# Kernel tuning notes

Measured on AMD Instinct MI355X. Metric: run time of the kernel, lower is better.

The kernel has to match this reference:

```python
import jax, jax.numpy as jnp
import numpy as np

NEG_SLOPE = 0.2  # PyG GATConv default negative_slope


def setup_inputs() -> dict:
    key = jax.random.key(0)
    ks = jax.random.split(key, 6)
    N, E, IN, H, C = 100000, 1600000, 128, 4, 32
    x = jax.random.normal(ks[0], (N, IN), dtype=jnp.float32)
    edge_index = jax.random.randint(ks[1], (2, E), 0, N, dtype=jnp.int64)
    W = jax.random.normal(ks[2], (IN, H * C), dtype=jnp.float32) * (1.0 / np.sqrt(IN))
    att_src = jax.random.normal(ks[3], (H, C), dtype=jnp.float32) * 0.1
    att_dst = jax.random.normal(ks[4], (H, C), dtype=jnp.float32) * 0.1
    bias = jax.random.normal(ks[5], (H * C,), dtype=jnp.float32) * 0.01
    return {"x": x, "edge_index": edge_index, "W": W,
            "att_src": att_src, "att_dst": att_dst, "bias": bias}


def reference(x, edge_index, W, att_src, att_dst, bias):
    N = x.shape[0]
    H, C = att_src.shape
    # PyG GATConv default add_self_loops=True
    loops = jnp.arange(N, dtype=edge_index.dtype)
    src = jnp.concatenate([edge_index[0], loops])  # [Et]
    dst = jnp.concatenate([edge_index[1], loops])  # [Et]
    # shared linear transform (GATConv uses one lin when in_channels is int)
    h = (x @ W).reshape(N, H, C)                   # [N,H,C]
    a_src = jnp.einsum('nhc,hc->nh', h, att_src)   # [N,H]
    a_dst = jnp.einsum('nhc,hc->nh', h, att_dst)   # [N,H]
    # edge attention logits + leaky relu
    e = jax.nn.leaky_relu(a_src[src] + a_dst[dst], NEG_SLOPE)  # [Et,H]
    # segment softmax over incoming edges of each destination node
    m = jax.ops.segment_max(e, dst, num_segments=N)            # [N,H]
    p = jnp.exp(e - m[dst])                                    # [Et,H]
    denom = jax.ops.segment_sum(p, dst, num_segments=N)        # [N,H]
    alpha = p / denom[dst]                                     # [Et,H]
    # weighted message passing: gather src features, scale, scatter-add to dst
    msg = h[src] * alpha[:, :, None]                           # [Et,H,C]
    out = jax.ops.segment_sum(msg, dst, num_segments=N)        # [N,H,C]
    out = out.reshape(N, H * C) + bias                         # concat heads + bias
    return jax.nn.elu(out)                                     # block ELU (dropout off)
```

## Files before the change

### kernel.cpp

```cpp
#include <hip/hip_runtime.h>
#include <hip/hip_bf16.h>

#define NEG_SLOPE 0.2f
#define BCAP 5120u

typedef __attribute__((ext_vector_type(8))) short bf16x8;
typedef __attribute__((ext_vector_type(4))) float f32x4;

__device__ __forceinline__ float lrelu(float v) { return v > 0.0f ? v : NEG_SLOPE * v; }

__device__ __forceinline__ unsigned bf16pair(float a, float b) {
    unsigned ua = __float_as_uint(a), ub = __float_as_uint(b);
    ua = (ua + 0x7FFFu + ((ua >> 16) & 1u)) >> 16;
    ub = (ub + 0x7FFFu + ((ub >> 16) & 1u)) >> 16;
    return ua | (ub << 16);
}

__device__ __forceinline__ void gload16(const void* g, void* l) {
    __builtin_amdgcn_global_load_lds(
        (const __attribute__((address_space(1))) unsigned*)g,
        (__attribute__((address_space(3))) unsigned*)l, 16, 0, 0);
}

__global__ __launch_bounds__(256) void k_wt(const float* __restrict__ W,
                                            unsigned short* __restrict__ Wt) {
    int gid = blockIdx.x * 256 + threadIdx.x;
    int col = gid >> 7, k = gid & 127;
    float v = W[(size_t)k * 128 + col];
    unsigned u = __float_as_uint(v);
    u = (u + 0x7FFFu + ((u >> 16) & 1u)) >> 16;
    Wt[col * 128 + k] = (unsigned short)u;
}

__global__ __launch_bounds__(512) void k_gembk(const float* __restrict__ x,
                                               const unsigned short* __restrict__ Wt,
                                               const float* __restrict__ att_src,
                                               const float* __restrict__ att_dst,
                                               unsigned* __restrict__ hb,
                                               float* __restrict__ a_src,
                                               float* __restrict__ a_dst,
                                               const int* __restrict__ ei,
                                               unsigned* __restrict__ gcur,
                                               unsigned* __restrict__ ebuf,
                                               int N, int E, int NB, int NBK, int EPB) {
    __shared__ unsigned char sm[65536];
    int t = threadIdx.x;

    if ((int)blockIdx.x < NBK) {
        unsigned* cnt = (unsigned*)sm;
        unsigned* cur2 = (unsigned*)(sm + 2048);
        unsigned* lbase = (unsigned*)(sm + 4096);
        int base = blockIdx.x * EPB;
        int lim = base + EPB;
        if (lim > E) lim = E;
        for (int j = t; j < NB; j += 512) { cnt[j] = 0u; cur2[j] = 0u; }
        __syncthreads();
        for (int i = base + t; i < lim; i += 512)
            atomicAdd(&cnt[(unsigned)ei[(size_t)E + i] >> 8], 1u);
        __syncthreads();
        for (int j = t; j < NB; j += 512) {
            unsigned c = cnt[j];
            lbase[j] = c ? ((unsigned)j * BCAP + atomicAdd(&gcur[j], c)) : 0u;
        }
        __syncthreads();
        for (int i = base + t; i < lim; i += 512) {
            unsigned s = (unsigned)ei[i];
            unsigned d = (unsigned)ei[(size_t)E + i];
            unsigned b = d >> 8;
            unsigned k = atomicAdd(&cur2[b], 1u);
            unsigned slot = lbase[b] + k;
            if (slot < (b + 1u) * BCAP) ebuf[slot] = s | ((d & 255u) << 24);
        }
        return;
    }

    unsigned char* smA = sm;
    unsigned char* smB = sm + 32768;
    int w = t >> 6, lane = t & 63;
    int row0 = ((int)blockIdx.x - NBK) * 128;

#pragma unroll
    for (int it = 0; it < 4; ++it) {
        int L = it * 512 + t;
        int r = L >> 4, c = L & 15;
        int gr = row0 + r;
        if (gr >= N) gr = N - 1;
        float4 f0 = ((const float4*)x)[(size_t)gr * 32 + c * 2];
        float4 f1 = ((const float4*)x)[(size_t)gr * 32 + c * 2 + 1];
        uint4 u;
        u.x = bf16pair(f0.x, f0.y);
        u.y = bf16pair(f0.z, f0.w);
        u.z = bf16pair(f1.x, f1.y);
        u.w = bf16pair(f1.z, f1.w);
        *(uint4*)&smA[r * 256 + ((c ^ (r & 7)) * 16)] = u;
    }
#pragma unroll
    for (int it = 0; it < 4; ++it) {
        int L = w * 256 + it * 64 + lane;
        int r = L >> 4, c = L & 15;
        int cg = c ^ (r & 7);
        gload16((const unsigned*)Wt + r * 64 + cg * 4, smB + (size_t)w * 4096 + it * 1024);
    }
    __syncthreads();

    int lr = lane & 15, lg = lane >> 4;
    int ar = w * 16 + lr;

    f32x4 acc[8];
#pragma unroll
    for (int j = 0; j < 8; ++j)
#pragma unroll
        for (int q = 0; q < 4; ++q) acc[j][q] = 0.f;

#pragma unroll
    for (int kc = 0; kc < 4; ++kc) {
        bf16x8 av = *(const bf16x8*)&smA[ar * 256 + (((kc * 4 + lg) ^ (ar & 7)) * 16)];
        bf16x8 bv[8];
#pragma unroll
        for (int cf = 0; cf < 8; ++cf) {
            int bc = cf * 16 + lr;
            bv[cf] = *(const bf16x8*)&smB[bc * 256 + (((kc * 4 + lg) ^ (bc & 7)) * 16)];
        }
#pragma unroll
        for (int cf = 0; cf < 8; ++cf)
            acc[cf] = __builtin_amdgcn_mfma_f32_16x16x32_bf16(av, bv[cf], acc[cf], 0, 0, 0);
    }

    float att_s[8], att_d[8];
#pragma unroll
    for (int cf = 0; cf < 8; ++cf) {
        att_s[cf] = att_src[cf * 16 + lr];
        att_d[cf] = att_dst[cf * 16 + lr];
    }
#pragma unroll
    for (int reg = 0; reg < 4; ++reg) {
        int row = row0 + w * 16 + lg * 4 + reg;
        float ps[4], pd[4];
#pragma unroll
        for (int hh = 0; hh < 4; ++hh) {
            ps[hh] = acc[2 * hh][reg] * att_s[2 * hh] + acc[2 * hh + 1][reg] * att_s[2 * hh + 1];
            pd[hh] = acc[2 * hh][reg] * att_d[2 * hh] + acc[2 * hh + 1][reg] * att_d[2 * hh + 1];
        }
#pragma unroll
        for (int m = 1; m <= 8; m <<= 1) {
#pragma unroll
            for (int hh = 0; hh < 4; ++hh) {
                ps[hh] += __shfl_xor(ps[hh], m);
                pd[hh] += __shfl_xor(pd[hh], m);
            }
        }
        if (lr == 0 && row < N) {
            ((float4*)a_src)[row] = float4{ps[0], ps[1], ps[2], ps[3]};
            ((float4*)a_dst)[row] = float4{pd[0], pd[1], pd[2], pd[3]};
        }
    }

    unsigned char* scratch = smA + (size_t)w * 4096;
#pragma unroll
    for (int cf = 0; cf < 8; ++cf) {
#pragma unroll
        for (int reg = 0; reg < 4; ++reg) {
            float v = acc[cf][reg];
            float vo = __shfl_xor(v, 1);
            if (!(lane & 1))
                *(unsigned*)&scratch[(lg * 4 + reg) * 256 + cf * 32 + (lr >> 1) * 4] =
                    bf16pair(v, vo);
        }
    }
#pragma unroll
    for (int q = 0; q < 4; ++q) {
        uint4 u = *(const uint4*)&scratch[q * 1024 + lane * 16];
        int row = row0 + w * 16 + q * 4 + lg;
        if (row < N) ((uint4*)hb)[(size_t)row * 16 + lr] = u;
    }
}

__global__ __launch_bounds__(512) void k_scanB(const unsigned* __restrict__ gcur,
                                               unsigned* __restrict__ blockScan, int NB) {
    __shared__ unsigned s[512];
    int t = threadIdx.x;
    unsigned v = (t < NB) ? min(gcur[t], BCAP) : 0u;
    s[t] = v;
    __syncthreads();
    for (int off = 1; off < 512; off <<= 1) {
        unsigned a = (t >= off) ? s[t - off] : 0u;
        __syncthreads();
        s[t] += a;
        __syncthreads();
    }
    if (t < NB) blockScan[t] = s[t] - v;
}

__global__ __launch_bounds__(256) void k_place(const unsigned* __restrict__ ebuf,
                                               const unsigned* __restrict__ gcur,
                                               const unsigned* __restrict__ blockScan,
                                               unsigned* __restrict__ deg,
                                               unsigned* __restrict__ part,
                                               unsigned* __restrict__ csr_src) {
    __shared__ unsigned cnt[256];
    __shared__ unsigned sc[256];
    __shared__ unsigned excl[256];
    __shared__ unsigned curL[256];
    int t = threadIdx.x;
    int b = blockIdx.x;
    cnt[t] = 0u;
    curL[t] = 0u;
    __syncthreads();
    unsigned total = min(gcur[b], BCAP);
    unsigned rbase = (unsigned)b * BCAP;
    for (unsigned i = t; i < total; i += 256)
        atomicAdd(&cnt[ebuf[rbase + i] >> 24], 1u);
    __syncthreads();
    unsigned v = cnt[t];
    sc[t] = v;
    __syncthreads();
    for (int off = 1; off < 256; off <<= 1) {
        unsigned a = (t >= off) ? sc[t - off] : 0u;
        __syncthreads();
        sc[t] += a;
        __syncthreads();
    }
    excl[t] = sc[t] - v;
    deg[b * 256 + t] = v;
    part[b * 256 + t] = sc[t] - v;
    __syncthreads();
    unsigned wbase = blockScan[b];
    for (unsigned i = t; i < total; i += 256) {
        unsigned e = ebuf[rbase + i];
        unsigned dLow = e >> 24;
        unsigned r = atomicAdd(&curL[dLow], 1u);
        csr_src[wbase + excl[dLow] + r] = e & 0x00FFFFFFu;
    }
}

__global__ __launch_bounds__(256) void k_gather(const uint4* __restrict__ hb4,
                                                const unsigned* __restrict__ csr_src,
                                                const unsigned* __restrict__ part,
                                                const unsigned* __restrict__ blockScan,
                                                const unsigned* __restrict__ deg,
                                                const float* __restrict__ a_src,
                                                const float* __restrict__ a_dst,
                                                const float* __restrict__ bias,
                                                float* __restrict__ out, int N) {
    int n = (int)((blockIdx.x * 256 + threadIdx.x) >> 6);
    int lane = threadIdx.x & 63;
    if (n >= N) return;
    int g = lane >> 4;
    int L = lane & 15;
    int head = L >> 2;
    unsigned off = part[n] + blockScan[n >> 8];
    unsigned end = off + deg[n];
    float ad_n = a_dst[n * 4 + head];
    float acc[8];
#pragma unroll
    for (int i = 0; i < 8; ++i) acc[i] = 0.f;
    float dsum = 0.f;
    for (unsigned b = off; b < end; b += 8) {
        unsigned sidx = csr_src[min(b + (unsigned)(lane & 7), end - 1)];
#pragma unroll
        for (int sub = 0; sub < 2; ++sub) {
            int eidx = sub * 4 + g;
            unsigned s = (unsigned)__shfl((int)sidx, eidx);
            float as = a_src[s * 4 + head];
            uint4 u = hb4[s * 16u + (unsigned)L];
            float p = __expf(lrelu(as + ad_n));
            p = (b + (unsigned)eidx < end) ? p : 0.f;
            acc[0] = fmaf(p, __uint_as_float(u.x << 16), acc[0]);
            acc[1] = fmaf(p, __uint_as_float(u.x & 0xFFFF0000u), acc[1]);
            acc[2] = fmaf(p, __uint_as_float(u.y << 16), acc[2]);
            acc[3] = fmaf(p, __uint_as_float(u.y & 0xFFFF0000u), acc[3]);
            acc[4] = fmaf(p, __uint_as_float(u.z << 16), acc[4]);
            acc[5] = fmaf(p, __uint_as_float(u.z & 0xFFFF0000u), acc[5]);
            acc[6] = fmaf(p, __uint_as_float(u.w << 16), acc[6]);
            acc[7] = fmaf(p, __uint_as_float(u.w & 0xFFFF0000u), acc[7]);
            dsum += p;
        }
    }
#pragma unroll
    for (int m = 16; m <= 32; m <<= 1) {
#pragma unroll
        for (int i = 0; i < 8; ++i) acc[i] += __shfl_xor(acc[i], m);
        dsum += __shfl_xor(dsum, m);
    }
    float p_self = __expf(lrelu(a_src[n * 4 + head] + ad_n));
    uint4 us = hb4[(unsigned)n * 16u + (unsigned)L];
    acc[0] = fmaf(p_self, __uint_as_float(us.x << 16), acc[0]);
    acc[1] = fmaf(p_self, __uint_as_float(us.x & 0xFFFF0000u), acc[1]);
    acc[2] = fmaf(p_self, __uint_as_float(us.y << 16), acc[2]);
    acc[3] = fmaf(p_self, __uint_as_float(us.y & 0xFFFF0000u), acc[3]);
    acc[4] = fmaf(p_self, __uint_as_float(us.z << 16), acc[4]);
    acc[5] = fmaf(p_self, __uint_as_float(us.z & 0xFFFF0000u), acc[5]);
    acc[6] = fmaf(p_self, __uint_as_float(us.w << 16), acc[6]);
    acc[7] = fmaf(p_self, __uint_as_float(us.w & 0xFFFF0000u), acc[7]);
    dsum += p_self;
    float inv = 1.0f / dsum;
    if (g == 0) {
        float4 b0 = ((const float4*)bias)[L * 2];
        float4 b1 = ((const float4*)bias)[L * 2 + 1];
        float4 o0, o1;
        o0.x = acc[0] * inv + b0.x;
        o0.y = acc[1] * inv + b0.y;
        o0.z = acc[2] * inv + b0.z;
        o0.w = acc[3] * inv + b0.w;
        o1.x = acc[4] * inv + b1.x;
        o1.y = acc[5] * inv + b1.y;
        o1.z = acc[6] * inv + b1.z;
        o1.w = acc[7] * inv + b1.w;
        o0.x = o0.x > 0.f ? o0.x : (__expf(o0.x) - 1.0f);
        o0.y = o0.y > 0.f ? o0.y : (__expf(o0.y) - 1.0f);
        o0.z = o0.z > 0.f ? o0.z : (__expf(o0.z) - 1.0f);
        o0.w = o0.w > 0.f ? o0.w : (__expf(o0.w) - 1.0f);
        o1.x = o1.x > 0.f ? o1.x : (__expf(o1.x) - 1.0f);
        o1.y = o1.y > 0.f ? o1.y : (__expf(o1.y) - 1.0f);
        o1.z = o1.z > 0.f ? o1.z : (__expf(o1.z) - 1.0f);
        o1.w = o1.w > 0.f ? o1.w : (__expf(o1.w) - 1.0f);
        ((float4*)out)[(size_t)n * 32 + L * 2] = o0;
        ((float4*)out)[(size_t)n * 32 + L * 2 + 1] = o1;
    }
}

extern "C" void kernel_launch(void* const* d_in, const int* in_sizes, int n_in,
                              void* d_out, int out_size, void* d_ws, size_t ws_size,
                              hipStream_t stream) {
    const float* x = (const float*)d_in[0];
    const int* ei = (const int*)d_in[1];
    const float* W = (const float*)d_in[2];
    const float* att_src = (const float*)d_in[3];
    const float* att_dst = (const float*)d_in[4];
    const float* bias = (const float*)d_in[5];
    int N = in_sizes[0] / 128;
    int E = in_sizes[1] / 2;
    int NB = (N + 255) / 256;

    char* ws = (char*)d_ws;
    size_t o = 0;
    unsigned* hb = (unsigned*)(ws + o);   o += (size_t)N * 64 * 4;
    float* a_src = (float*)(ws + o);      o += (size_t)N * 4 * 4;
    float* a_dst = (float*)(ws + o);      o += (size_t)N * 4 * 4;
    unsigned* csr_src = (unsigned*)(ws + o); o += (size_t)E * 4;
    unsigned* ebuf = (unsigned*)(ws + o); o += (size_t)NB * BCAP * 4;
    unsigned short* Wt = (unsigned short*)(ws + o); o += 128 * 128 * 2;
    unsigned* deg = (unsigned*)(ws + o);  o += (size_t)NB * 256 * 4;
    unsigned* part = (unsigned*)(ws + o); o += (size_t)NB * 256 * 4;
    unsigned* gcur = (unsigned*)(ws + o); o += 2048;
    unsigned* blockScan = (unsigned*)(ws + o); o += 2048;

    hipMemsetAsync(gcur, 0, 2048, stream);

    k_wt<<<64, 256, 0, stream>>>(W, Wt);
    int EPB = 16384;
    int NBK = (E + EPB - 1) / EPB;
    int nbG = (N + 127) / 128;
    k_gembk<<<NBK + nbG, 512, 0, stream>>>(x, Wt, att_src, att_dst, hb, a_src, a_dst,
                                           ei, gcur, ebuf, N, E, NB, NBK, EPB);
    k_scanB<<<1, 512, 0, stream>>>(gcur, blockScan, NB);
    k_place<<<NB, 256, 0, stream>>>(ebuf, gcur, blockScan, deg, part, csr_src);
    k_gather<<<(N * 64 + 255) / 256, 256, 0, stream>>>((const uint4*)hb, csr_src, part,
                                                       blockScan, deg, a_src, a_dst, bias,
                                                       (float*)d_out, N);
}
```

Baseline: 147.5 us.

## Drop scan kernel and memset by using padded per-bucket CSR layout

Removes the single-block prefix-scan kernel by laying out csr_src with a fixed BCAP stride per destination bucket, so offsets come from bucket index times BCAP instead of a global scan. The gcur memset is folded into the W-transpose kernel. The bucketing phase now caches destination indices in LDS to avoid re-reading them from global memory, and edges per block are halved so more blocks share the work. The padded CSR costs more workspace and produces a sparser layout.

```diff
diff --git a/kernel.cpp b/kernel.cpp
--- a/kernel.cpp
+++ b/kernel.cpp
@@ -23,8 +23,14 @@
 }
 
 __global__ __launch_bounds__(256) void k_wt(const float* __restrict__ W,
-                                            unsigned short* __restrict__ Wt) {
-    int gid = blockIdx.x * 256 + threadIdx.x;
+                                            unsigned short* __restrict__ Wt,
+                                            unsigned* __restrict__ gcur) {
+    int t = threadIdx.x;
+    if (blockIdx.x == 0) {
+        gcur[t] = 0u;
+        gcur[t + 256] = 0u;
+    }
+    int gid = blockIdx.x * 256 + t;
     int col = gid >> 7, k = gid & 127;
     float v = W[(size_t)k * 128 + col];
     unsigned u = __float_as_uint(v);
@@ -47,25 +53,30 @@
     int t = threadIdx.x;
 
     if ((int)blockIdx.x < NBK) {
-        unsigned* cnt = (unsigned*)sm;
-        unsigned* cur2 = (unsigned*)(sm + 2048);
-        unsigned* lbase = (unsigned*)(sm + 4096);
+        unsigned* dstbuf = (unsigned*)sm;
+        unsigned* cnt = (unsigned*)(sm + 32768);
+        unsigned* cur2 = (unsigned*)(sm + 34816);
+        unsigned* lbase = (unsigned*)(sm + 36864);
         int base = blockIdx.x * EPB;
         int lim = base + EPB;
         if (lim > E) lim = E;
+        int n_sl = lim - base;
         for (int j = t; j < NB; j += 512) { cnt[j] = 0u; cur2[j] = 0u; }
         __syncthreads();
-        for (int i = base + t; i < lim; i += 512)
-            atomicAdd(&cnt[(unsigned)ei[(size_t)E + i] >> 8], 1u);
+        for (int i = t; i < n_sl; i += 512) {
+            unsigned d = (unsigned)ei[(size_t)E + base + i];
+            dstbuf[i] = d;
+            atomicAdd(&cnt[d >> 8], 1u);
+        }
         __syncthreads();
         for (int j = t; j < NB; j += 512) {
             unsigned c = cnt[j];
             lbase[j] = c ? ((unsigned)j * BCAP + atomicAdd(&gcur[j], c)) : 0u;
         }
         __syncthreads();
-        for (int i = base + t; i < lim; i += 512) {
-            unsigned s = (unsigned)ei[i];
-            unsigned d = (unsigned)ei[(size_t)E + i];
+        for (int i = t; i < n_sl; i += 512) {
+            unsigned s = (unsigned)ei[base + i];
+            unsigned d = dstbuf[i];
             unsigned b = d >> 8;
             unsigned k = atomicAdd(&cur2[b], 1u);
             unsigned slot = lbase[b] + k;
@@ -175,25 +186,8 @@
     }
 }
 
-__global__ __launch_bounds__(512) void k_scanB(const unsigned* __restrict__ gcur,
-                                               unsigned* __restrict__ blockScan, int NB) {
-    __shared__ unsigned s[512];
-    int t = threadIdx.x;
-    unsigned v = (t < NB) ? min(gcur[t], BCAP) : 0u;
-    s[t] = v;
-    __syncthreads();
-    for (int off = 1; off < 512; off <<= 1) {
-        unsigned a = (t >= off) ? s[t - off] : 0u;
-        __syncthreads();
-        s[t] += a;
-        __syncthreads();
-    }
-    if (t < NB) blockScan[t] = s[t] - v;
-}
-
 __global__ __launch_bounds__(256) void k_place(const unsigned* __restrict__ ebuf,
                                                const unsigned* __restrict__ gcur,
-                                               const unsigned* __restrict__ blockScan,
                                                unsigned* __restrict__ deg,
                                                unsigned* __restrict__ part,
                                                unsigned* __restrict__ csr_src) {
@@ -224,19 +218,17 @@
     deg[b * 256 + t] = v;
     part[b * 256 + t] = sc[t] - v;
     __syncthreads();
-    unsigned wbase = blockScan[b];
     for (unsigned i = t; i < total; i += 256) {
         unsigned e = ebuf[rbase + i];
         unsigned dLow = e >> 24;
         unsigned r = atomicAdd(&curL[dLow], 1u);
-        csr_src[wbase + excl[dLow] + r] = e & 0x00FFFFFFu;
+        csr_src[rbase + excl[dLow] + r] = e & 0x00FFFFFFu;
     }
 }
 
 __global__ __launch_bounds__(256) void k_gather(const uint4* __restrict__ hb4,
                                                 const unsigned* __restrict__ csr_src,
                                                 const unsigned* __restrict__ part,
-                                                const unsigned* __restrict__ blockScan,
                                                 const unsigned* __restrict__ deg,
                                                 const float* __restrict__ a_src,
                                                 const float* __restrict__ a_dst,
@@ -248,7 +240,7 @@
     int g = lane >> 4;
     int L = lane & 15;
     int head = L >> 2;
-    unsigned off = part[n] + blockScan[n >> 8];
+    unsigned off = (unsigned)(n >> 8) * BCAP + part[n];
     unsigned end = off + deg[n];
     float ad_n = a_dst[n * 4 + head];
     float acc[8];
@@ -337,25 +329,21 @@
     unsigned* hb = (unsigned*)(ws + o);   o += (size_t)N * 64 * 4;
     float* a_src = (float*)(ws + o);      o += (size_t)N * 4 * 4;
     float* a_dst = (float*)(ws + o);      o += (size_t)N * 4 * 4;
-    unsigned* csr_src = (unsigned*)(ws + o); o += (size_t)E * 4;
+    unsigned* csr_src = (unsigned*)(ws + o); o += (size_t)NB * BCAP * 4;
     unsigned* ebuf = (unsigned*)(ws + o); o += (size_t)NB * BCAP * 4;
     unsigned short* Wt = (unsigned short*)(ws + o); o += 128 * 128 * 2;
     unsigned* deg = (unsigned*)(ws + o);  o += (size_t)NB * 256 * 4;
     unsigned* part = (unsigned*)(ws + o); o += (size_t)NB * 256 * 4;
     unsigned* gcur = (unsigned*)(ws + o); o += 2048;
-    unsigned* blockScan = (unsigned*)(ws + o); o += 2048;
-
-    hipMemsetAsync(gcur, 0, 2048, stream);
-
-    k_wt<<<64, 256, 0, stream>>>(W, Wt);
-    int EPB = 16384;
+
+    k_wt<<<64, 256, 0, stream>>>(W, Wt, gcur);
+    int EPB = 8192;
     int NBK = (E + EPB - 1) / EPB;
     int nbG = (N + 127) / 128;
     k_gembk<<<NBK + nbG, 512, 0, stream>>>(x, Wt, att_src, att_dst, hb, a_src, a_dst,
                                            ei, gcur, ebuf, N, E, NB, NBK, EPB);
-    k_scanB<<<1, 512, 0, stream>>>(gcur, blockScan, NB);
-    k_place<<<NB, 256, 0, stream>>>(ebuf, gcur, blockScan, deg, part, csr_src);
+    k_place<<<NB, 256, 0, stream>>>(ebuf, gcur, deg, part, csr_src);
     k_gather<<<(N * 64 + 255) / 256, 256, 0, stream>>>((const uint4*)hb, csr_src, part,
-                                                       blockScan, deg, a_src, a_dst, bias,
+                                                       deg, a_src, a_dst, bias,
                                                        (float*)d_out, N);
 }
```

Result: faster. 139.8 us (-5.2%).
